# Kernel tuning notes

Hardware: AMD Instinct MI355X
Metric: run time of the kernel (lower is better)

The kernel has to match this reference:

```python
import jax, jax.numpy as jnp
import numpy as np

D_MODEL = 1024
D_STATE = 16
D_CONV = 4
EXPAND = 2
D_INNER = EXPAND * D_MODEL          # 2048
DT_RANK = (D_MODEL + 15) // 16      # 64
BSZ, T0, H0, W0 = 4, 8, 16, 16
SEQLEN = T0 * H0 * W0               # 2048
N_BANDS = 8


def setup_inputs() -> dict:
    key = jax.random.key(0)
    ks = jax.random.split(key, 8)
    hidden_states = jax.random.normal(ks[0], (BSZ, SEQLEN, D_MODEL), jnp.float32)
    in_proj_w = jax.random.normal(ks[1], (2 * D_INNER, D_MODEL), jnp.float32) * (D_MODEL ** -0.5)
    conv_w = jax.random.normal(ks[2], (D_INNER, 1, D_CONV), jnp.float32) * (D_CONV ** -0.5)
    conv_b = jnp.zeros((D_INNER,), jnp.float32)
    x_proj_w = jax.random.normal(ks[3], (DT_RANK + 2 * D_STATE, D_INNER), jnp.float32) * (D_INNER ** -0.5)
    dt_std = DT_RANK ** -0.5
    dt_proj_w = jax.random.uniform(ks[4], (D_INNER, DT_RANK), jnp.float32, -dt_std, dt_std)
    # inverse-softplus init of dt bias, as in the torch module
    dt = jnp.exp(jax.random.uniform(ks[5], (D_INNER,), jnp.float32)
                 * (np.log(0.1) - np.log(0.001)) + np.log(0.001))
    dt = jnp.clip(dt, 1e-4, None)
    dt_proj_b = dt + jnp.log(-jnp.expm1(-dt))
    A_log = jnp.log(jnp.tile(jnp.arange(1, D_STATE + 1, dtype=jnp.float32)[None, :], (D_INNER, 1)))
    D_param = jnp.ones((D_INNER,), jnp.float32)
    out_proj_w = jax.random.normal(ks[6], (D_MODEL, D_INNER), jnp.float32) * (D_INNER ** -0.5)
    return dict(hidden_states=hidden_states, T=T0, H=H0, W=W0,
                in_proj_w=in_proj_w, conv_w=conv_w, conv_b=conv_b,
                x_proj_w=x_proj_w, dt_proj_w=dt_proj_w, dt_proj_b=dt_proj_b,
                A_log=A_log, D=D_param, out_proj_w=out_proj_w)


def _channel_alignment(x, B, T, H, W):
    """x: (B, C, L=T*H*W) -> (align_loss scalar, features (B*T, C))."""
    C = x.shape[1]
    x4 = x.reshape(B, C, T, H, W).transpose(0, 2, 1, 3, 4).reshape(B * T, C, H, W)
    fr = jnp.fft.rfft2(x4, axes=(-2, -1))
    mag = jnp.sqrt(fr.real ** 2 + fr.imag ** 2 + 1e-8)
    mag = jnp.fft.fftshift(mag, axes=(-2, -1))
    Wr = mag.shape[-1]                      # W//2 + 1
    hg = jnp.arange(H)[:, None]
    wg = jnp.arange(Wr)[None, :]
    r = jnp.sqrt(((hg - H // 2) / H) ** 2 + ((wg - Wr // 2) / Wr) ** 2)
    masks = jnp.stack([((r >= i / N_BANDS) & (r < (i + 1) / N_BANDS)).astype(mag.dtype)
                       for i in range(N_BANDS)])          # (8, H, Wr)
    bands = jnp.einsum('bchw,khw->bck', mag, masks)        # (B*T, C, 8)
    bands = bands / (bands.sum(-1, keepdims=True) + 1e-8)
    features = bands[..., N_BANDS // 2:].sum(-1)           # (B*T, C) high-freq ratio
    fn = features / jnp.maximum(jnp.linalg.norm(features, axis=1, keepdims=True), 1e-12)
    sim = fn @ fn.T
    Bt = features.shape[0]
    loss = 1.0 - sim.sum() / (Bt * Bt)
    return loss, features


def _invert_A(A_log, features):
    """Blend A_log toward its column-flipped version, weighted by channel features."""
    A_max = A_log.max(axis=0, keepdims=True)
    A_min = A_log.min(axis=0, keepdims=True)
    A_flipped = A_max + A_min - A_log
    attention = jnp.linalg.norm(jnp.exp(A_log), axis=1)
    attention = attention / (attention.max() + 1e-8)
    f = jax.nn.softmax(jax.lax.stop_gradient(features).mean(axis=0))
    alpha = jnp.clip(f * (1.0 - attention), 0.0, 1.0)[:, None]   # (d_inner, 1)
    return (1.0 - alpha) * A_log + alpha * A_flipped


def reference(hidden_states, T, H, W, in_proj_w, conv_w, conv_b,
              x_proj_w, dt_proj_w, dt_proj_b, A_log, D, out_proj_w):
    B, L, _ = hidden_states.shape
    xz = jnp.einsum('bld,ed->bel', hidden_states, in_proj_w)      # (B, 2*d_inner, L)
    x, z = xz[:, :D_INNER], xz[:, D_INNER:]

    align_loss, features = _channel_alignment(x, B, T, H, W)
    A_log_new = _invert_A(A_log, features)
    A = -jnp.exp(A_log_new)                                       # (d_inner, d_state)

    # causal depthwise conv1d + SiLU (left pad d_conv-1 == torch pad then slice :L)
    xc = jax.lax.conv_general_dilated(x, conv_w, (1,), [(D_CONV - 1, 0)],
                                      dimension_numbers=('NCH', 'OIH', 'NCH'),
                                      feature_group_count=D_INNER)
    xc = jax.nn.silu(xc + conv_b[None, :, None])                  # (B, d_inner, L)

    x_dbl = jnp.einsum('bdl,ed->ble', xc, x_proj_w)               # (B, L, dt_rank+2N)
    dt_low = x_dbl[..., :DT_RANK]
    Bm = x_dbl[..., DT_RANK:DT_RANK + D_STATE]                    # (B, L, N)
    Cm = x_dbl[..., DT_RANK + D_STATE:]                           # (B, L, N)
    delta = jax.nn.softplus(jnp.einsum('blr,dr->bld', dt_low, dt_proj_w) + dt_proj_b)

    u = xc.transpose(0, 2, 1)                                     # (B, L, d_inner)

    def step(s, inp):
        d_t, u_t, B_t, C_t = inp                                  # (B,D),(B,D),(B,N),(B,N)
        s = s * jnp.exp(d_t[..., None] * A) + (d_t * u_t)[..., None] * B_t[:, None, :]
        y_t = jnp.einsum('bdn,bn->bd', s, C_t)
        return s, y_t

    s0 = jnp.zeros((B, D_INNER, D_STATE), delta.dtype)
    _, ys = jax.lax.scan(step, s0,
                         (delta.transpose(1, 0, 2), u.transpose(1, 0, 2),
                          Bm.transpose(1, 0, 2), Cm.transpose(1, 0, 2)))
    y = ys.transpose(1, 0, 2)                                     # (B, L, d_inner)
    y = y + u * D
    y = y * jax.nn.silu(z.transpose(0, 2, 1))
    out = jnp.einsum('bld,ed->ble', y, out_proj_w)                # (B, L, d_model)
    return out, align_loss
```

## Files before the change

kernel.cpp:

```cpp
#include <hip/hip_runtime.h>
#include <math.h>
#include <stdint.h>

#define LSEQ 2048
#define DM   1024
#define DI   2048
#define NC   32
#define CL   64

#define OFF_X     ((size_t)0)
#define OFF_Z     ((size_t)16777216)
#define OFF_U     ((size_t)33554432)
#define OFF_S     ((size_t)50331648)
#define OFF_CS    (OFF_S)
#define OFF_SDT   (OFF_S + 4194304)
#define OFF_XDBL  (OFF_S + 4456448)
#define OFF_FEAT  (OFF_S + 5242880)
#define OFF_AWS   (OFF_S + 5308448)
#define OFF_B1    ((size_t)58720256)

__device__ __forceinline__ float silu_(float x) { return x / (1.f + __expf(-x)); }
__device__ __forceinline__ float softplus_(float x) {
  return fmaxf(x, 0.f) + log1pf(__expf(-fabsf(x)));
}
__device__ __forceinline__ unsigned short f2bf(float x) {
  unsigned int u = __float_as_uint(x);
  u += 0x7fffu + ((u >> 16) & 1u);
  return (unsigned short)(u >> 16);
}
__device__ __forceinline__ float bf2f(unsigned short h) {
  return __uint_as_float(((unsigned int)h) << 16);
}

typedef __attribute__((ext_vector_type(8))) short bf16x8;
typedef __attribute__((ext_vector_type(4))) float f32x4;

__device__ __forceinline__ void gl2lds16(const void* g, void* l) {
  __builtin_amdgcn_global_load_lds(
      (const __attribute__((address_space(1))) unsigned int*)(uintptr_t)g,
      (__attribute__((address_space(3))) unsigned int*)(uintptr_t)l,
      16, 0, 0);
}

#define BARRIER_()                                   \
  do {                                               \
    asm volatile("" ::: "memory");                   \
    __builtin_amdgcn_s_barrier();                    \
    asm volatile("" ::: "memory");                   \
  } while (0)

__global__ __launch_bounds__(256) void split2_w(
    const float* __restrict__ a, unsigned short* __restrict__ oa, int ksa,
    size_t na4,
    const float* __restrict__ b, unsigned short* __restrict__ ob, int ksb)
{
  size_t i4 = ((size_t)blockIdx.x << 8) + threadIdx.x;
  const float* src; unsigned short* dst; int ks;
  if (i4 < na4) { src = a; dst = oa; ks = ksa; }
  else          { src = b; dst = ob; ks = ksb; i4 -= na4; }
  const size_t flat = i4 << 2;
  const int K = 1 << ks;
  const size_t row = flat >> ks;
  const int k = (int)(flat & (size_t)(K - 1));
  float4 v = *(const float4*)(src + flat);
  float f[4] = {v.x, v.y, v.z, v.w};
  unsigned short h[4], lo[4];
#pragma unroll
  for (int c = 0; c < 4; ++c) { h[c] = f2bf(f[c]); lo[c] = f2bf(f[c] - bf2f(h[c])); }
  unsigned short* o = dst + (row << (ks + 1)) + k;
  *(uint2*)(o)     = make_uint2((unsigned)h[0]  | ((unsigned)h[1]  << 16),
                                (unsigned)h[2]  | ((unsigned)h[3]  << 16));
  *(uint2*)(o + K) = make_uint2((unsigned)lo[0] | ((unsigned)lo[1] << 16),
                                (unsigned)lo[2] | ((unsigned)lo[3] << 16));
}

template <int NPASS, int MH, int NH>
__device__ __forceinline__ void phase_mfma(
    const unsigned short* __restrict__ shc, f32x4 (&acc)[8][4],
    int wm, int wn, int lm, int roff)
{
  bf16x8 aH[4], bH[2], aL[4], bL[2];
#pragma unroll
  for (int ii = 0; ii < 4; ++ii) {
    const int ar = (wm + (MH * 4 + ii) * 16 + lm) * 32 + roff;
    aH[ii] = *(const bf16x8*)(shc + ar);
    if constexpr (NPASS > 1) aL[ii] = *(const bf16x8*)(shc + 2 * 8192 + ar);
  }
#pragma unroll
  for (int jj = 0; jj < 2; ++jj) {
    const int br = (wn + (NH * 2 + jj) * 16 + lm) * 32 + roff;
    bH[jj] = *(const bf16x8*)(shc + 8192 + br);
    if constexpr (NPASS > 1) bL[jj] = *(const bf16x8*)(shc + 3 * 8192 + br);
  }
  __builtin_amdgcn_s_setprio(1);
#pragma unroll
  for (int ii = 0; ii < 4; ++ii)
#pragma unroll
    for (int jj = 0; jj < 2; ++jj) {
      const int i = MH * 4 + ii, j = NH * 2 + jj;
      acc[i][j] = __builtin_amdgcn_mfma_f32_16x16x32_bf16(aH[ii], bH[jj], acc[i][j], 0, 0, 0);
      if constexpr (NPASS > 1) {
        acc[i][j] = __builtin_amdgcn_mfma_f32_16x16x32_bf16(aH[ii], bL[jj], acc[i][j], 0, 0, 0);
        acc[i][j] = __builtin_amdgcn_mfma_f32_16x16x32_bf16(aL[ii], bH[jj], acc[i][j], 0, 0, 0);
      }
    }
  __builtin_amdgcn_s_setprio(0);
}

template <int NPASS>
__global__ __launch_bounds__(512, 2) void gemm_8ph(
    const unsigned short* __restrict__ Ap, const unsigned short* __restrict__ Bp,
    float* __restrict__ C, int K, int ldc)
{
  constexpr int NTEN = (NPASS > 1) ? 4 : 2;
  __shared__ unsigned short sh[2][NTEN][256 * 32];
  const int tid = threadIdx.x;
  const int bn = blockIdx.x << 8;
  const int bm = blockIdx.y << 8;
  const int K2 = K * 2;
  const int wave = tid >> 6, lane = tid & 63;
  const int wm = (wave >> 2) << 7;
  const int wn = (wave & 3) << 6;
  const int lm = lane & 15, quad = lane >> 4;
  const int roff = ((quad ^ ((lm >> 1) & 3)) << 3);

  const int r0 = tid >> 2;
  const int kq = (((tid & 3) ^ ((r0 >> 1) & 3)) << 3);
  const unsigned short* a0 = Ap + (size_t)(bm + r0) * K2 + kq;
  const unsigned short* a1 = a0 + (size_t)128 * K2;
  const unsigned short* b0 = Bp + (size_t)(bn + r0) * K2 + kq;
  const unsigned short* b1 = b0 + (size_t)128 * K2;
  const int ls0 = tid * 8, ls1 = 4096 + tid * 8;

  f32x4 acc[8][4] = {};
  const int NT = K >> 5;

  {
    unsigned short* s = &sh[0][0][0];
    gl2lds16(a0, s + ls0);
    gl2lds16(a1, s + ls1);
    if constexpr (NPASS > 1) {
      gl2lds16(a0 + K, s + 2 * 8192 + ls0);
      gl2lds16(a1 + K, s + 2 * 8192 + ls1);
    }
    gl2lds16(b0, s + 8192 + ls0);
    gl2lds16(b1, s + 8192 + ls1);
    if constexpr (NPASS > 1) {
      gl2lds16(b0 + K, s + 3 * 8192 + ls0);
      gl2lds16(b1 + K, s + 3 * 8192 + ls1);
    }
  }

  for (int t = 0; t < NT - 1; ++t) {
    const unsigned short* cur = &sh[t & 1][0][0];
    unsigned short* nxt = &sh[(t + 1) & 1][0][0];
    const int kn = (t + 1) << 5;

    gl2lds16(a0 + kn, nxt + ls0);
    gl2lds16(a1 + kn, nxt + ls1);
    if constexpr (NPASS > 1) {
      gl2lds16(a0 + K + kn, nxt + 2 * 8192 + ls0);
      gl2lds16(a1 + K + kn, nxt + 2 * 8192 + ls1);
      asm volatile("s_waitcnt vmcnt(4)" ::: "memory");
    } else {
      asm volatile("s_waitcnt vmcnt(2)" ::: "memory");
    }
    BARRIER_();
    phase_mfma<NPASS, 0, 0>(cur, acc, wm, wn, lm, roff);
    BARRIER_();
    gl2lds16(b0 + kn, nxt + 8192 + ls0);
    gl2lds16(b1 + kn, nxt + 8192 + ls1);
    if constexpr (NPASS > 1) {
      gl2lds16(b0 + K + kn, nxt + 3 * 8192 + ls0);
      gl2lds16(b1 + K + kn, nxt + 3 * 8192 + ls1);
    }
    phase_mfma<NPASS, 0, 1>(cur, acc, wm, wn, lm, roff);
    BARRIER_();
    phase_mfma<NPASS, 1, 0>(cur, acc, wm, wn, lm, roff);
    BARRIER_();
    phase_mfma<NPASS, 1, 1>(cur, acc, wm, wn, lm, roff);
    BARRIER_();
  }

  {
    const unsigned short* cur = &sh[(NT - 1) & 1][0][0];
    asm volatile("s_waitcnt vmcnt(0)" ::: "memory");
    BARRIER_();
    phase_mfma<NPASS, 0, 0>(cur, acc, wm, wn, lm, roff);
    BARRIER_();
    phase_mfma<NPASS, 0, 1>(cur, acc, wm, wn, lm, roff);
    BARRIER_();
    phase_mfma<NPASS, 1, 0>(cur, acc, wm, wn, lm, roff);
    BARRIER_();
    phase_mfma<NPASS, 1, 1>(cur, acc, wm, wn, lm, roff);
  }

#pragma unroll
  for (int i = 0; i < 8; ++i) {
    const int m = bm + wm + i * 16 + quad * 4;
#pragma unroll
    for (int j = 0; j < 4; ++j) {
      const int n = bn + wn + j * 16 + lm;
#pragma unroll
      for (int r = 0; r < 4; ++r)
        C[(size_t)(m + r) * ldc + n] = acc[i][j][r];
    }
  }
}

template <int MH, int NH>
__device__ __forceinline__ void phase8(
    const unsigned short* __restrict__ ah, const unsigned short* __restrict__ al,
    const unsigned short* __restrict__ bh, const unsigned short* __restrict__ bl,
    f32x4 (&acc)[8][2], int wm, int wn, int lm, int roff)
{
  bf16x8 aH[4], aL[4];
#pragma unroll
  for (int ii = 0; ii < 4; ++ii) {
    const int ar = (wm + (MH * 4 + ii) * 16 + lm) * 32 + roff;
    aH[ii] = *(const bf16x8*)(ah + ar);
    aL[ii] = *(const bf16x8*)(al + ar);
  }
  const int br = (wn + NH * 16 + lm) * 32 + roff;
  bf16x8 bH = *(const bf16x8*)(bh + br);
  bf16x8 bL = *(const bf16x8*)(bl + br);
  __builtin_amdgcn_s_setprio(1);
#pragma unroll
  for (int ii = 0; ii < 4; ++ii) {
    const int i = MH * 4 + ii;
    acc[i][NH] = __builtin_amdgcn_mfma_f32_16x16x32_bf16(aH[ii], bH, acc[i][NH], 0, 0, 0);
    acc[i][NH] = __builtin_amdgcn_mfma_f32_16x16x32_bf16(aH[ii], bL, acc[i][NH], 0, 0, 0);
    acc[i][NH] = __builtin_amdgcn_mfma_f32_16x16x32_bf16(aL[ii], bH, acc[i][NH], 0, 0, 0);
  }
  __builtin_amdgcn_s_setprio(0);
}

__global__ __launch_bounds__(512, 2) void gemm8_8ph(
    const unsigned int* __restrict__ Ay,
    const unsigned short* __restrict__ Bp,
    float* __restrict__ C)
{
  constexpr int K = 2048, K2 = 4096, ldc = 1024;
  __shared__ unsigned short AHs[2][256 * 32];
  __shared__ unsigned short ALs[2][256 * 32];
  __shared__ unsigned short BHs[2][128 * 32];
  __shared__ unsigned short BLs[2][128 * 32];
  const int tid = threadIdx.x;
  const int bn = blockIdx.x << 7;
  const int bm = blockIdx.y << 8;
  const int wave = tid >> 6, lane = tid & 63;
  const int wm = (wave >> 2) << 7;
  const int wn = (wave & 3) << 5;
  const int lm = lane & 15, quad = lane >> 4;
  const int roff = ((quad ^ ((lm >> 1) & 3)) << 3);

  const int ra = tid >> 1;
  const int g0 = (tid & 1) << 1;
  const int aswz = (ra >> 1) & 3;
  const int sa0 = (ra * 32) + ((g0 ^ aswz) << 3);
  const int sa1 = (ra * 32) + (((g0 + 1) ^ aswz) << 3);
  const unsigned int* ag = Ay + (size_t)(bm + ra) * K + (g0 << 3);

  const int rb = tid >> 2;
  const int kqb = (((tid & 3) ^ ((rb >> 1) & 3)) << 3);
  const unsigned short* bg = Bp + (size_t)(bn + rb) * K2 + kqb;
  const int lsb = tid * 8;

  f32x4 acc[8][2] = {};
  constexpr int NT = K / 32;

  uint4 w0, w1, w2, w3;
#define LOADA_(kn) do { const unsigned int* p_ = ag + (kn);               \
    w0 = *(const uint4*)p_;        w1 = *(const uint4*)(p_ + 4);          \
    w2 = *(const uint4*)(p_ + 8);  w3 = *(const uint4*)(p_ + 12); } while (0)
#define WRITEA_(bufi) do {                                                \
    unsigned h0 = (w0.x & 0xffffu) | (w0.y << 16);                        \
    unsigned h1 = (w0.z & 0xffffu) | (w0.w << 16);                        \
    unsigned h2 = (w1.x & 0xffffu) | (w1.y << 16);                        \
    unsigned h3 = (w1.z & 0xffffu) | (w1.w << 16);                        \
    unsigned h4 = (w2.x & 0xffffu) | (w2.y << 16);                        \
    unsigned h5 = (w2.z & 0xffffu) | (w2.w << 16);                        \
    unsigned h6 = (w3.x & 0xffffu) | (w3.y << 16);                        \
    unsigned h7 = (w3.z & 0xffffu) | (w3.w << 16);                        \
    unsigned l0 = (w0.x >> 16) | (w0.y & 0xffff0000u);                    \
    unsigned l1 = (w0.z >> 16) | (w0.w & 0xffff0000u);                    \
    unsigned l2 = (w1.x >> 16) | (w1.y & 0xffff0000u);                    \
    unsigned l3 = (w1.z >> 16) | (w1.w & 0xffff0000u);                    \
    unsigned l4 = (w2.x >> 16) | (w2.y & 0xffff0000u);                    \
    unsigned l5 = (w2.z >> 16) | (w2.w & 0xffff0000u);                    \
    unsigned l6 = (w3.x >> 16) | (w3.y & 0xffff0000u);                    \
    unsigned l7 = (w3.z >> 16) | (w3.w & 0xffff0000u);                    \
    *(uint4*)&AHs[bufi][sa0] = make_uint4(h0, h1, h2, h3);                \
    *(uint4*)&AHs[bufi][sa1] = make_uint4(h4, h5, h6, h7);                \
    *(uint4*)&ALs[bufi][sa0] = make_uint4(l0, l1, l2, l3);                \
    *(uint4*)&ALs[bufi][sa1] = make_uint4(l4, l5, l6, l7); } while (0)

  LOADA_(0);
  gl2lds16(bg,     &BHs[0][lsb]);
  gl2lds16(bg + K, &BLs[0][lsb]);
  asm volatile("s_waitcnt vmcnt(2)" ::: "memory");
  WRITEA_(0);
  asm volatile("s_waitcnt lgkmcnt(0)" ::: "memory");

  for (int t = 0; t < NT - 1; ++t) {
    const int cb = t & 1, nb = cb ^ 1;
    const int kn = (t + 1) << 5;
    LOADA_(kn);
    asm volatile("s_waitcnt vmcnt(4)" ::: "memory");
    BARRIER_();
    phase8<0, 0>(AHs[cb], ALs[cb], BHs[cb], BLs[cb], acc, wm, wn, lm, roff);
    BARRIER_();
    gl2lds16(bg + kn,     &BHs[nb][lsb]);
    gl2lds16(bg + K + kn, &BLs[nb][lsb]);
    phase8<0, 1>(AHs[cb], ALs[cb], BHs[cb], BLs[cb], acc, wm, wn, lm, roff);
    BARRIER_();
    asm volatile("s_waitcnt vmcnt(2)" ::: "memory");
    WRITEA_(nb);
    phase8<1, 0>(AHs[cb], ALs[cb], BHs[cb], BLs[cb], acc, wm, wn, lm, roff);
    BARRIER_();
    phase8<1, 1>(AHs[cb], ALs[cb], BHs[cb], BLs[cb], acc, wm, wn, lm, roff);
    asm volatile("s_waitcnt lgkmcnt(0)" ::: "memory");
    BARRIER_();
  }

  {
    const int cb = (NT - 1) & 1;
    asm volatile("s_waitcnt vmcnt(0)" ::: "memory");
    BARRIER_();
    phase8<0, 0>(AHs[cb], ALs[cb], BHs[cb], BLs[cb], acc, wm, wn, lm, roff);
    BARRIER_();
    phase8<0, 1>(AHs[cb], ALs[cb], BHs[cb], BLs[cb], acc, wm, wn, lm, roff);
    BARRIER_();
    phase8<1, 0>(AHs[cb], ALs[cb], BHs[cb], BLs[cb], acc, wm, wn, lm, roff);
    BARRIER_();
    phase8<1, 1>(AHs[cb], ALs[cb], BHs[cb], BLs[cb], acc, wm, wn, lm, roff);
  }
#undef LOADA_
#undef WRITEA_

#pragma unroll
  for (int i = 0; i < 8; ++i) {
    const int m = bm + wm + i * 16 + quad * 4;
#pragma unroll
    for (int j = 0; j < 2; ++j) {
      const int n = bn + wn + j * 16 + lm;
#pragma unroll
      for (int r = 0; r < 4; ++r)
        C[(size_t)(m + r) * ldc + n] = acc[i][j][r];
    }
  }
}

template <int EPI>
__global__ __launch_bounds__(256) void gemm_nt(
    const float* __restrict__ A, int lda,
    const float* __restrict__ B, int ldb,
    float* __restrict__ C, int ldc,
    int N, int K, const float* __restrict__ bias, size_t cseg)
{
  __shared__ float As[16][68];
  __shared__ float Bs[16][68];
  const int tid = threadIdx.x;
  const int bm = blockIdx.y << 6;
  const int bn = blockIdx.x << 6;
  const int kz = blockIdx.z;
  A += (size_t)kz * K;
  B += (size_t)kz * K;
  C += (size_t)kz * cseg;
  const int lr = tid >> 2;
  const int lk = (tid & 3) << 2;
  const int tx = tid & 15, ty = tid >> 4;

  float acc[4][4];
#pragma unroll
  for (int i = 0; i < 4; ++i)
#pragma unroll
    for (int j = 0; j < 4; ++j) acc[i][j] = 0.f;

  const float* Apt = A + (size_t)(bm + lr) * lda + lk;
  const float* Bpt = B + (size_t)(bn + lr) * ldb + lk;
  const bool bv = (bn + lr) < N;

  for (int k0 = 0; k0 < K; k0 += 16) {
    float4 a4 = *(const float4*)(Apt + k0);
    float4 b4 = bv ? *(const float4*)(Bpt + k0) : make_float4(0.f, 0.f, 0.f, 0.f);
    __syncthreads();
    As[lk + 0][lr] = a4.x; As[lk + 1][lr] = a4.y;
    As[lk + 2][lr] = a4.z; As[lk + 3][lr] = a4.w;
    Bs[lk + 0][lr] = b4.x; Bs[lk + 1][lr] = b4.y;
    Bs[lk + 2][lr] = b4.z; Bs[lk + 3][lr] = b4.w;
    __syncthreads();
#pragma unroll
    for (int k = 0; k < 16; ++k) {
      const float4 av = *(const float4*)(&As[k][ty << 2]);
      const float4 bw = *(const float4*)(&Bs[k][tx << 2]);
      float a4r[4] = {av.x, av.y, av.z, av.w};
      float b4r[4] = {bw.x, bw.y, bw.z, bw.w};
#pragma unroll
      for (int i = 0; i < 4; ++i)
#pragma unroll
        for (int j = 0; j < 4; ++j)
          acc[i][j] = fmaf(a4r[i], b4r[j], acc[i][j]);
    }
  }

  const int m = bm + (ty << 2);
  const int n = bn + (tx << 2);
#pragma unroll
  for (int i = 0; i < 4; ++i) {
    float v[4] = {acc[i][0], acc[i][1], acc[i][2], acc[i][3]};
    if (EPI == 1) {
#pragma unroll
      for (int j = 0; j < 4; ++j)
        if (n + j < N) v[j] = softplus_(v[j] + bias[n + j]);
    }
    if (n + 3 < N) {
      *(float4*)(C + (size_t)(m + i) * ldc + n) = make_float4(v[0], v[1], v[2], v[3]);
    } else {
#pragma unroll
      for (int j = 0; j < 4; ++j)
        if (n + j < N) C[(size_t)(m + i) * ldc + n + j] = v[j];
    }
  }
}

__global__ __launch_bounds__(256) void reduce4(
    const float* __restrict__ P, float* __restrict__ O, size_t seg)
{
  const size_t i = ((size_t)blockIdx.x << 8) + threadIdx.x;
  float4 a = ((const float4*)P)[i];
  float4 b = ((const float4*)(P + seg))[i];
  float4 c = ((const float4*)(P + 2 * seg))[i];
  float4 d = ((const float4*)(P + 3 * seg))[i];
  ((float4*)O)[i] = make_float4(a.x + b.x + c.x + d.x,
                                a.y + b.y + c.y + d.y,
                                a.z + b.z + c.z + d.z,
                                a.w + b.w + c.w + d.w);
}

__global__ __launch_bounds__(256) void feat_kernel(
    const float* __restrict__ X, float* __restrict__ features)
{
  __shared__ float xin[256][17];
  __shared__ float Rf[16 * 315];
  __shared__ float tc[16], ts[16];
  __shared__ float part2[16][16][2];

  const int tid = threadIdx.x;
  const int frame = blockIdx.x >> 7;
  const int cg = blockIdx.x & 127;
  const int b = frame >> 3, t = frame & 7;
  const int c0 = cg << 4;

  if (tid < 16) {
    float ang = 0.39269908169872414f * (float)tid;
    tc[tid] = cosf(ang);
    ts[tid] = sinf(ang);
  }
  const float* xb = X + ((size_t)(b * LSEQ + t * 256) << 11) + c0;
  for (int i = tid; i < 256 * 16; i += 256) {
    int hw = i >> 4, ci = i & 15;
    xin[hw][ci] = xb[((size_t)hw << 11) + ci];
  }
  __syncthreads();

  {
    const int ci = tid & 15, h = tid >> 4;
    float re[9], im[9];
#pragma unroll
    for (int kw = 0; kw < 9; ++kw) { re[kw] = 0.f; im[kw] = 0.f; }
#pragma unroll
    for (int w = 0; w < 16; ++w) {
      float x = xin[(h << 4) + w][ci];
#pragma unroll
      for (int kw = 0; kw < 9; ++kw) {
        int ph = (kw * w) & 15;
        re[kw] = fmaf(x, tc[ph], re[kw]);
        im[kw] = fmaf(-x, ts[ph], im[kw]);
      }
    }
#pragma unroll
    for (int kw = 0; kw < 9; ++kw) {
      Rf[ci * 315 + kw * 35 + 2 * h]     = re[kw];
      Rf[ci * 315 + kw * 35 + 2 * h + 1] = im[kw];
    }
  }
  __syncthreads();

  {
    const int ci = tid & 15, kh = tid >> 4;
    float ut = 0.f, tt = 0.f;
    for (int kw = 0; kw < 9; ++kw) {
      float fre = 0.f, fim = 0.f;
#pragma unroll
      for (int h = 0; h < 16; ++h) {
        int ph = (kh * h) & 15;
        float c = tc[ph], s = ts[ph];
        float rr = Rf[ci * 315 + kw * 35 + 2 * h];
        float ri = Rf[ci * 315 + kw * 35 + 2 * h + 1];
        fre += rr * c + ri * s;
        fim += ri * c - rr * s;
      }
      float mag = sqrtf(fre * fre + fim * fim + 1e-8f);
      int sh = (kh + 8) & 15;
      int sw2 = kw + 4; if (sw2 >= 9) sw2 -= 9;
      float dh = (float)(sh - 8) / 16.0f;
      float dw = (float)(sw2 - 4) / 9.0f;
      tt += mag;
      if (dh * dh + dw * dw >= 0.25f) ut += mag;
    }
    part2[ci][kh][0] = ut;
    part2[ci][kh][1] = tt;
  }
  __syncthreads();

  if (tid < 16) {
    float ut = 0.f, tt = 0.f;
    for (int kh = 0; kh < 16; ++kh) { ut += part2[tid][kh][0]; tt += part2[tid][kh][1]; }
    features[frame * DI + c0 + tid] = ut / (tt + 1e-8f);
  }
}

__global__ __launch_bounds__(256) void alpha_kernel(
    const float* __restrict__ feats, const float* __restrict__ A_log,
    float* __restrict__ Aws, float* __restrict__ loss_out)
{
  __shared__ float red[256];
  __shared__ float invn[32];
  __shared__ float PT[32][257];
  __shared__ float AM[256][17];
  __shared__ float sAmax[16], sAmin[16];
  const int tid = threadIdx.x;

  float pn[32];
#pragma unroll
  for (int i = 0; i < 32; ++i) pn[i] = 0.f;
  float md[8];
#pragma unroll
  for (int j = 0; j < 8; ++j) md[j] = 0.f;
  for (int i = 0; i < 32; ++i) {
#pragma unroll
    for (int j = 0; j < 8; ++j) {
      float v = feats[(i << 11) + tid + (j << 8)];
      pn[i] = fmaf(v, v, pn[i]);
      md[j] += v;
    }
  }
#pragma unroll
  for (int j = 0; j < 8; ++j) md[j] *= (1.f / 32.f);
#pragma unroll
  for (int i = 0; i < 32; ++i) PT[i][tid] = pn[i];
  __syncthreads();
  if (tid < 32) {
    float s = 0.f;
    for (int k = 0; k < 256; ++k) s += PT[tid][k];
    invn[tid] = 1.f / fmaxf(sqrtf(s), 1e-12f);
  }
  __syncthreads();

  float gsq = 0.f;
#pragma unroll
  for (int j = 0; j < 8; ++j) {
    float gd = 0.f;
    for (int i = 0; i < 32; ++i)
      gd = fmaf(feats[(i << 11) + tid + (j << 8)], invn[i], gd);
    gsq = fmaf(gd, gd, gsq);
  }
  red[tid] = gsq; __syncthreads();
  for (int s = 128; s > 0; s >>= 1) { if (tid < s) red[tid] += red[tid + s]; __syncthreads(); }
  if (tid == 0) loss_out[0] = 1.f - red[0] * (1.f / 1024.f);
  __syncthreads();

  float lm = md[0];
#pragma unroll
  for (int j = 1; j < 8; ++j) lm = fmaxf(lm, md[j]);
  red[tid] = lm; __syncthreads();
  for (int s = 128; s > 0; s >>= 1) { if (tid < s) red[tid] = fmaxf(red[tid], red[tid + s]); __syncthreads(); }
  const float mmax = red[0]; __syncthreads();

  float p[8]; float ps = 0.f;
#pragma unroll
  for (int j = 0; j < 8; ++j) { p[j] = __expf(md[j] - mmax); ps += p[j]; }
  red[tid] = ps; __syncthreads();
  for (int s = 128; s > 0; s >>= 1) { if (tid < s) red[tid] += red[tid + s]; __syncthreads(); }
  const float psum = red[0]; __syncthreads();

  float amaxl[16], aminl[16], rn[8];
#pragma unroll
  for (int n = 0; n < 16; ++n) { amaxl[n] = -1e30f; aminl[n] = 1e30f; }
#pragma unroll
  for (int j = 0; j < 8; ++j) {
    const int d = tid + (j << 8);
    float ss = 0.f;
#pragma unroll
    for (int n = 0; n < 16; ++n) {
      float a = A_log[(d << 4) + n];
      float e = __expf(a);
      ss = fmaf(e, e, ss);
      amaxl[n] = fmaxf(amaxl[n], a);
      aminl[n] = fminf(aminl[n], a);
    }
    rn[j] = sqrtf(ss);
  }
  float rm = rn[0];
#pragma unroll
  for (int j = 1; j < 8; ++j) rm = fmaxf(rm, rn[j]);
  red[tid] = rm; __syncthreads();
  for (int s = 128; s > 0; s >>= 1) { if (tid < s) red[tid] = fmaxf(red[tid], red[tid + s]); __syncthreads(); }
  const float rnmax = red[0]; __syncthreads();

#pragma unroll
  for (int n = 0; n < 16; ++n) AM[tid][n] = amaxl[n];
  __syncthreads();
  if (tid < 16) { float m = -1e30f; for (int i = 0; i < 256; ++i) m = fmaxf(m, AM[i][tid]); sAmax[tid] = m; }
  __syncthreads();
#pragma unroll
  for (int n = 0; n < 16; ++n) AM[tid][n] = aminl[n];
  __syncthreads();
  if (tid < 16) { float m = 1e30f; for (int i = 0; i < 256; ++i) m = fminf(m, AM[i][tid]); sAmin[tid] = m; }
  __syncthreads();

  const float irn = 1.f / (rnmax + 1e-8f);
#pragma unroll
  for (int j = 0; j < 8; ++j) {
    const int d = tid + (j << 8);
    const float att = rn[j] * irn;
    const float f = p[j] / psum;
    const float alpha = fminf(fmaxf(f * (1.f - att), 0.f), 1.f);
#pragma unroll
    for (int n = 0; n < 16; ++n) {
      float a = A_log[(d << 4) + n];
      float fl = sAmax[n] + sAmin[n] - a;
      float an = (1.f - alpha) * a + alpha * fl;
      Aws[(d << 4) + n] = -__expf(an) * 1.4426950408889634f;
    }
  }
}

__global__ __launch_bounds__(256) void conv_kernel(
    const float* __restrict__ X, const float* __restrict__ cw,
    const float* __restrict__ cb, float* __restrict__ U)
{
  const size_t i4 = ((size_t)blockIdx.x << 8) + threadIdx.x;
  const int e4 = (int)(i4 & 511);
  const size_t row = i4 >> 9;
  const int l = (int)(row & 2047);
  const float* xr = X + (row << 11) + (e4 << 2);
  const float4 z4 = make_float4(0.f, 0.f, 0.f, 0.f);
  float4 x0 = *(const float4*)xr;
  float4 x1 = (l >= 1) ? *(const float4*)(xr - 2048) : z4;
  float4 x2 = (l >= 2) ? *(const float4*)(xr - 4096) : z4;
  float4 x3 = (l >= 3) ? *(const float4*)(xr - 6144) : z4;
  const float4* cwf = (const float4*)cw;
  float4 bi = *(const float4*)(cb + (e4 << 2));
  float x0a[4] = {x0.x, x0.y, x0.z, x0.w};
  float x1a[4] = {x1.x, x1.y, x1.z, x1.w};
  float x2a[4] = {x2.x, x2.y, x2.z, x2.w};
  float x3a[4] = {x3.x, x3.y, x3.z, x3.w};
  float bia[4] = {bi.x, bi.y, bi.z, bi.w};
  float o[4];
#pragma unroll
  for (int c = 0; c < 4; ++c) {
    float4 w = cwf[(e4 << 2) + c];
    float acc = bia[c];
    acc = fmaf(x3a[c], w.x, acc);
    acc = fmaf(x2a[c], w.y, acc);
    acc = fmaf(x1a[c], w.z, acc);
    acc = fmaf(x0a[c], w.w, acc);
    o[c] = silu_(acc);
  }
  *(float4*)(U + (i4 << 2)) = make_float4(o[0], o[1], o[2], o[3]);
}

__global__ __launch_bounds__(256) void scan_pass1(
    const float* __restrict__ delta, const float* __restrict__ U,
    const float* __restrict__ xdbl, const float* __restrict__ Aws,
    float* __restrict__ cs, float* __restrict__ sdt)
{
  __shared__ float blds[CL * 16];
  const int tid = threadIdx.x;
  const int dg = blockIdx.x & 7;
  const int chunk = (blockIdx.x >> 3) & 31;
  const int b = blockIdx.x >> 8;
  const int d = (dg << 8) | tid;
  const int l0 = chunk * CL;

  for (int i = tid; i < CL * 16; i += 256) {
    int l = i >> 4, j = i & 15;
    blds[i] = xdbl[(size_t)(b * LSEQ + l0 + l) * 96 + 64 + j];
  }
  __syncthreads();

  float Ar[16];
#pragma unroll
  for (int n = 0; n < 16; ++n) Ar[n] = Aws[(d << 4) + n];
  float s[16];
#pragma unroll
  for (int n = 0; n < 16; ++n) s[n] = 0.f;
  float sumdt = 0.f;

  const float* dp = delta + ((size_t)b << 22) + ((size_t)l0 << 11) + d;
  const float* up = U + ((size_t)b << 22) + ((size_t)l0 << 11) + d;

  for (int l = 0; l < CL; ++l) {
    const float dt = dp[(size_t)l << 11];
    const float u = up[(size_t)l << 11];
    sumdt += dt;
    const float du = dt * u;
    const float* bl = &blds[l << 4];
#pragma unroll
    for (int n = 0; n < 16; ++n)
      s[n] = fmaf(s[n], __builtin_amdgcn_exp2f(dt * Ar[n]), du * bl[n]);
  }

  float* csp = cs + ((((size_t)b * NC + chunk) * 2048 + d) << 4);
#pragma unroll
  for (int n = 0; n < 4; ++n)
    *(float4*)(csp + (n << 2)) = make_float4(s[4*n], s[4*n+1], s[4*n+2], s[4*n+3]);
  sdt[((size_t)b * NC + chunk) * 2048 + d] = sumdt;
}

__global__ __launch_bounds__(256) void scan_mid(
    float* __restrict__ cs, const float* __restrict__ sdt,
    const float* __restrict__ Aws)
{
  const int b = blockIdx.x >> 3;
  const int d = ((blockIdx.x & 7) << 8) | threadIdx.x;
  float Ar[16];
#pragma unroll
  for (int n = 0; n < 16; ++n) Ar[n] = Aws[(d << 4) + n];
  float si[16];
#pragma unroll
  for (int n = 0; n < 16; ++n) si[n] = 0.f;

  for (int c = 0; c < NC; ++c) {
    const size_t base = ((size_t)b * NC + c) * 2048 + d;
    float* csp = cs + (base << 4);
    float sl[16];
#pragma unroll
    for (int n = 0; n < 4; ++n) {
      float4 v = *(const float4*)(csp + (n << 2));
      sl[4*n] = v.x; sl[4*n+1] = v.y; sl[4*n+2] = v.z; sl[4*n+3] = v.w;
    }
    const float sm = sdt[base];
#pragma unroll
    for (int n = 0; n < 4; ++n)
      *(float4*)(csp + (n << 2)) = make_float4(si[4*n], si[4*n+1], si[4*n+2], si[4*n+3]);
#pragma unroll
    for (int n = 0; n < 16; ++n)
      si[n] = fmaf(si[n], __builtin_amdgcn_exp2f(sm * Ar[n]), sl[n]);
  }
}

__global__ __launch_bounds__(256) void scan_pass3(
    const float* __restrict__ delta, const float* __restrict__ Z,
    float* __restrict__ U,
    const float* __restrict__ xdbl, const float* __restrict__ Aws,
    const float* __restrict__ Dp, const float* __restrict__ cs)
{
  __shared__ float bclds[CL * 32];
  const int tid = threadIdx.x;
  const int dg = blockIdx.x & 7;
  const int chunk = (blockIdx.x >> 3) & 31;
  const int b = blockIdx.x >> 8;
  const int d = (dg << 8) | tid;
  const int l0 = chunk * CL;

  for (int i = tid; i < CL * 32; i += 256) {
    int l = i >> 5, j = i & 31;
    bclds[i] = xdbl[(size_t)(b * LSEQ + l0 + l) * 96 + 64 + j];
  }
  __syncthreads();

  float Ar[16];
#pragma unroll
  for (int n = 0; n < 16; ++n) Ar[n] = Aws[(d << 4) + n];
  const float Dd = Dp[d];

  const float* csp = cs + ((((size_t)b * NC + chunk) * 2048 + d) << 4);
  float s[16];
#pragma unroll
  for (int n = 0; n < 4; ++n) {
    float4 v = *(const float4*)(csp + (n << 2));
    s[4*n] = v.x; s[4*n+1] = v.y; s[4*n+2] = v.z; s[4*n+3] = v.w;
  }

  const float* dp = delta + ((size_t)b << 22) + ((size_t)l0 << 11) + d;
  const float* zp = Z + ((size_t)b << 22) + ((size_t)l0 << 11) + d;
  float* up = U + ((size_t)b << 22) + ((size_t)l0 << 11) + d;

  for (int l = 0; l < CL; ++l) {
    const float dt = dp[(size_t)l << 11];
    const float u = up[(size_t)l << 11];
    const float z = zp[(size_t)l << 11];
    const float du = dt * u;
    const float* bcl = &bclds[l << 5];
    float y = 0.f;
#pragma unroll
    for (int n = 0; n < 16; ++n) {
      s[n] = fmaf(s[n], __builtin_amdgcn_exp2f(dt * Ar[n]), du * bcl[n]);
      y = fmaf(s[n], bcl[16 + n], y);
    }
    const float yv = fmaf(u, Dd, y);
    const float yo = yv * silu_(z);
    const unsigned short h = f2bf(yo);
    const unsigned short lo = f2bf(yo - bf2f(h));
    ((unsigned int*)up)[(size_t)l << 11] = (unsigned)h | ((unsigned)lo << 16);
  }
}

extern "C" void kernel_launch(void* const* d_in, const int* in_sizes, int n_in,
                              void* d_out, int out_size, void* d_ws, size_t ws_size,
                              hipStream_t stream)
{
  const float* hs         = (const float*)d_in[0];
  const float* in_proj_w  = (const float*)d_in[4];
  const float* conv_w     = (const float*)d_in[5];
  const float* conv_b     = (const float*)d_in[6];
  const float* x_proj_w   = (const float*)d_in[7];
  const float* dt_proj_w  = (const float*)d_in[8];
  const float* dt_proj_b  = (const float*)d_in[9];
  const float* A_log      = (const float*)d_in[10];
  const float* Dp         = (const float*)d_in[11];
  const float* out_proj_w = (const float*)d_in[12];
  float* out = (float*)d_out;
  float* ws = (float*)d_ws;

  float* X     = ws + OFF_X;
  float* Z     = ws + OFF_Z;
  float* U     = ws + OFF_U;
  float* cs    = ws + OFF_CS;
  float* sdt   = ws + OFF_SDT;
  float* xdbl  = ws + OFF_XDBL;
  float* feats = ws + OFF_FEAT;
  float* Aws   = ws + OFF_AWS;
  unsigned short* A1s = (unsigned short*)(ws + OFF_S);
  unsigned short* B1s = (unsigned short*)(ws + OFF_B1);
  unsigned short* B2s = (unsigned short*)(ws + OFF_B1);

  const dim3 blk(256);

  split2_w<<<12288, blk, 0, stream>>>(hs, A1s, 10, (size_t)2097152,
                                      in_proj_w, B1s, 10);
  gemm_8ph<3><<<dim3(8, 32), dim3(512), 0, stream>>>(A1s, B1s, X, 1024, 2048);
  gemm_8ph<1><<<dim3(8, 32), dim3(512), 0, stream>>>(A1s, B1s + (size_t)2048 * 2048, Z, 1024, 2048);
  feat_kernel<<<4096, blk, 0, stream>>>(X, feats);
  conv_kernel<<<16384, blk, 0, stream>>>(X, conv_w, conv_b, U);
  split2_w<<<2048, blk, 0, stream>>>(out_proj_w, B2s, 11, (size_t)524288,
                                     out_proj_w, B2s, 11);
  alpha_kernel<<<1, blk, 0, stream>>>(feats, A_log, Aws, out + 8388608);
  gemm_nt<0><<<dim3(2, 128, 4), blk, 0, stream>>>(U, DI, x_proj_w, DI, cs, 96, 96, 512, nullptr, (size_t)786432);
  reduce4<<<768, blk, 0, stream>>>(cs, xdbl, (size_t)786432);
  gemm_nt<1><<<dim3(32, 128, 1), blk, 0, stream>>>(xdbl, 96, dt_proj_w, 64, X, DI, DI, 64, dt_proj_b, 0);
  scan_pass1<<<1024, blk, 0, stream>>>(X, U, xdbl, Aws, cs, sdt);
  scan_mid<<<32, blk, 0, stream>>>(cs, sdt, Aws);
  scan_pass3<<<1024, blk, 0, stream>>>(X, Z, U, xdbl, Aws, Dp, cs);
  gemm8_8ph<<<dim3(8, 32), dim3(512), 0, stream>>>((const unsigned int*)U, B2s, out);
}
```

Before: 880.5 us.

## Deepen A-prefetch to two tiles and merge gemm8 phases into two per k-step

After: 900.2 us. 1.02x slower.

```diff
diff --git a/kernel.cpp b/kernel.cpp
--- a/kernel.cpp
+++ b/kernel.cpp
@@ -208,30 +208,35 @@
   }
 }
 
-template <int MH, int NH>
-__device__ __forceinline__ void phase8(
+template <int MH>
+__device__ __forceinline__ void phaseM8(
     const unsigned short* __restrict__ ah, const unsigned short* __restrict__ al,
     const unsigned short* __restrict__ bh, const unsigned short* __restrict__ bl,
     f32x4 (&acc)[8][2], int wm, int wn, int lm, int roff)
 {
-  bf16x8 aH[4], aL[4];
+  bf16x8 aH[4], aL[4], bH[2], bL[2];
 #pragma unroll
   for (int ii = 0; ii < 4; ++ii) {
     const int ar = (wm + (MH * 4 + ii) * 16 + lm) * 32 + roff;
     aH[ii] = *(const bf16x8*)(ah + ar);
     aL[ii] = *(const bf16x8*)(al + ar);
   }
-  const int br = (wn + NH * 16 + lm) * 32 + roff;
-  bf16x8 bH = *(const bf16x8*)(bh + br);
-  bf16x8 bL = *(const bf16x8*)(bl + br);
+#pragma unroll
+  for (int jj = 0; jj < 2; ++jj) {
+    const int br = (wn + jj * 16 + lm) * 32 + roff;
+    bH[jj] = *(const bf16x8*)(bh + br);
+    bL[jj] = *(const bf16x8*)(bl + br);
+  }
   __builtin_amdgcn_s_setprio(1);
 #pragma unroll
-  for (int ii = 0; ii < 4; ++ii) {
-    const int i = MH * 4 + ii;
-    acc[i][NH] = __builtin_amdgcn_mfma_f32_16x16x32_bf16(aH[ii], bH, acc[i][NH], 0, 0, 0);
-    acc[i][NH] = __builtin_amdgcn_mfma_f32_16x16x32_bf16(aH[ii], bL, acc[i][NH], 0, 0, 0);
-    acc[i][NH] = __builtin_amdgcn_mfma_f32_16x16x32_bf16(aL[ii], bH, acc[i][NH], 0, 0, 0);
-  }
+  for (int ii = 0; ii < 4; ++ii)
+#pragma unroll
+    for (int jj = 0; jj < 2; ++jj) {
+      const int i = MH * 4 + ii;
+      acc[i][jj] = __builtin_amdgcn_mfma_f32_16x16x32_bf16(aH[ii], bH[jj], acc[i][jj], 0, 0, 0);
+      acc[i][jj] = __builtin_amdgcn_mfma_f32_16x16x32_bf16(aH[ii], bL[jj], acc[i][jj], 0, 0, 0);
+      acc[i][jj] = __builtin_amdgcn_mfma_f32_16x16x32_bf16(aL[ii], bH[jj], acc[i][jj], 0, 0, 0);
+    }
   __builtin_amdgcn_s_setprio(0);
 }
 
@@ -240,7 +245,7 @@
     const unsigned short* __restrict__ Bp,
     float* __restrict__ C)
 {
-  constexpr int K = 2048, K2 = 4096, ldc = 1024;
+  constexpr int K = 2048, K2 = 4096, ldc = 1024, NT = 64;
   __shared__ unsigned short AHs[2][256 * 32];
   __shared__ unsigned short ALs[2][256 * 32];
   __shared__ unsigned short BHs[2][128 * 32];
@@ -267,13 +272,12 @@
   const int lsb = tid * 8;
 
   f32x4 acc[8][2] = {};
-  constexpr int NT = K / 32;
-
-  uint4 w0, w1, w2, w3;
-#define LOADA_(kn) do { const unsigned int* p_ = ag + (kn);               \
-    w0 = *(const uint4*)p_;        w1 = *(const uint4*)(p_ + 4);          \
-    w2 = *(const uint4*)(p_ + 8);  w3 = *(const uint4*)(p_ + 12); } while (0)
-#define WRITEA_(bufi) do {                                                \
+  uint4 r0a, r0b, r0c, r0d, r1a, r1b, r1c, r1d;
+
+#define LOADA_(d0, d1, d2, d3, kn) do {                                   \
+    const uint4* p_ = (const uint4*)(ag + (kn));                          \
+    d0 = p_[0]; d1 = p_[1]; d2 = p_[2]; d3 = p_[3]; } while (0)
+#define WRITEA_(bufi, w0, w1, w2, w3) do {                                \
     unsigned h0 = (w0.x & 0xffffu) | (w0.y << 16);                        \
     unsigned h1 = (w0.z & 0xffffu) | (w0.w << 16);                        \
     unsigned h2 = (w1.x & 0xffffu) | (w1.y << 16);                        \
@@ -295,48 +299,53 @@
     *(uint4*)&ALs[bufi][sa0] = make_uint4(l0, l1, l2, l3);                \
     *(uint4*)&ALs[bufi][sa1] = make_uint4(l4, l5, l6, l7); } while (0)
 
-  LOADA_(0);
+#define BODY_(t, Ca, Cb, Cc, Cd, Na, Nb_, Nc, Nd, cb, nb) do {            \
+    LOADA_(Ca, Cb, Cc, Cd, ((t) + 2) << 5);                               \
+    gl2lds16(bg + (((t) + 1) << 5),     &BHs[nb][lsb]);                   \
+    gl2lds16(bg + K + (((t) + 1) << 5), &BLs[nb][lsb]);                   \
+    asm volatile("s_waitcnt vmcnt(6)" ::: "memory");                      \
+    BARRIER_();                                                           \
+    phaseM8<0>(AHs[cb], ALs[cb], BHs[cb], BLs[cb], acc, wm, wn, lm, roff);\
+    BARRIER_();                                                           \
+    WRITEA_(nb, Na, Nb_, Nc, Nd);                                         \
+    phaseM8<1>(AHs[cb], ALs[cb], BHs[cb], BLs[cb], acc, wm, wn, lm, roff);\
+    asm volatile("s_waitcnt lgkmcnt(0)" ::: "memory");                    \
+    BARRIER_();                                                           \
+  } while (0)
+
+  LOADA_(r0a, r0b, r0c, r0d, 0);
   gl2lds16(bg,     &BHs[0][lsb]);
   gl2lds16(bg + K, &BLs[0][lsb]);
+  LOADA_(r1a, r1b, r1c, r1d, 32);
+  asm volatile("s_waitcnt vmcnt(4)" ::: "memory");
+  WRITEA_(0, r0a, r0b, r0c, r0d);
+  asm volatile("s_waitcnt lgkmcnt(0)" ::: "memory");
+  BARRIER_();
+
+  for (int t = 0; t + 3 < NT; t += 2) {
+    BODY_(t,     r0a, r0b, r0c, r0d, r1a, r1b, r1c, r1d, 0, 1);
+    BODY_(t + 1, r1a, r1b, r1c, r1d, r0a, r0b, r0c, r0d, 1, 0);
+  }
+
+  gl2lds16(bg + ((NT - 1) << 5),     &BHs[1][lsb]);
+  gl2lds16(bg + K + ((NT - 1) << 5), &BLs[1][lsb]);
   asm volatile("s_waitcnt vmcnt(2)" ::: "memory");
-  WRITEA_(0);
+  BARRIER_();
+  phaseM8<0>(AHs[0], ALs[0], BHs[0], BLs[0], acc, wm, wn, lm, roff);
+  BARRIER_();
+  WRITEA_(1, r1a, r1b, r1c, r1d);
+  phaseM8<1>(AHs[0], ALs[0], BHs[0], BLs[0], acc, wm, wn, lm, roff);
   asm volatile("s_waitcnt lgkmcnt(0)" ::: "memory");
-
-  for (int t = 0; t < NT - 1; ++t) {
-    const int cb = t & 1, nb = cb ^ 1;
-    const int kn = (t + 1) << 5;
-    LOADA_(kn);
-    asm volatile("s_waitcnt vmcnt(4)" ::: "memory");
-    BARRIER_();
-    phase8<0, 0>(AHs[cb], ALs[cb], BHs[cb], BLs[cb], acc, wm, wn, lm, roff);
-    BARRIER_();
-    gl2lds16(bg + kn,     &BHs[nb][lsb]);
-    gl2lds16(bg + K + kn, &BLs[nb][lsb]);
-    phase8<0, 1>(AHs[cb], ALs[cb], BHs[cb], BLs[cb], acc, wm, wn, lm, roff);
-    BARRIER_();
-    asm volatile("s_waitcnt vmcnt(2)" ::: "memory");
-    WRITEA_(nb);
-    phase8<1, 0>(AHs[cb], ALs[cb], BHs[cb], BLs[cb], acc, wm, wn, lm, roff);
-    BARRIER_();
-    phase8<1, 1>(AHs[cb], ALs[cb], BHs[cb], BLs[cb], acc, wm, wn, lm, roff);
-    asm volatile("s_waitcnt lgkmcnt(0)" ::: "memory");
-    BARRIER_();
-  }
-
-  {
-    const int cb = (NT - 1) & 1;
-    asm volatile("s_waitcnt vmcnt(0)" ::: "memory");
-    BARRIER_();
-    phase8<0, 0>(AHs[cb], ALs[cb], BHs[cb], BLs[cb], acc, wm, wn, lm, roff);
-    BARRIER_();
-    phase8<0, 1>(AHs[cb], ALs[cb], BHs[cb], BLs[cb], acc, wm, wn, lm, roff);
-    BARRIER_();
-    phase8<1, 0>(AHs[cb], ALs[cb], BHs[cb], BLs[cb], acc, wm, wn, lm, roff);
-    BARRIER_();
-    phase8<1, 1>(AHs[cb], ALs[cb], BHs[cb], BLs[cb], acc, wm, wn, lm, roff);
-  }
+  BARRIER_();
+  asm volatile("s_waitcnt vmcnt(0)" ::: "memory");
+  BARRIER_();
+  phaseM8<0>(AHs[1], ALs[1], BHs[1], BLs[1], acc, wm, wn, lm, roff);
+  BARRIER_();
+  phaseM8<1>(AHs[1], ALs[1], BHs[1], BLs[1], acc, wm, wn, lm, roff);
+
 #undef LOADA_
 #undef WRITEA_
+#undef BODY_
 
 #pragma unroll
   for (int i = 0; i < 8; ++i) {
```
